# Optimization experiments

Hardware: AMD Instinct MI355X
Metric: run time of the kernel (lower is better)

## Reference

```python
import jax, jax.numpy as jnp
import numpy as np

B, S, D = 8, 2048, 512


def setup_inputs() -> dict:
    key = jax.random.key(0)
    ks = jax.random.split(key, 11)
    scale = 1.0 / np.sqrt(D)
    inp = {"x": jax.random.normal(ks[0], (B, S, D), dtype=jnp.float32)}
    names = ["q", "k", "v", "g", "o"]
    for i, n in enumerate(names):
        inp[f"W{n}"] = jax.random.normal(ks[1 + 2 * i], (D, D), dtype=jnp.float32) * scale
        inp[f"b{n}"] = jax.random.normal(ks[2 + 2 * i], (D,), dtype=jnp.float32) * 0.01
    return inp


def reference(x, Wq, bq, Wk, bk, Wv, bv, Wg, bg, Wo, bo):
    # Projections (torch nn.Linear: x @ W.T + b)
    Q = x @ Wq.T + bq            # (B,S,D)
    K = x @ Wk.T + bk
    V = x @ Wv.T + bv
    gamma = jax.nn.sigmoid(x @ Wg.T + bg)

    # Recurrent linear-attention scan over time.
    # State St: (B,D,D); update: St = gamma_t[:, :, None] * St + k_t ⊗ v_t
    # (decay broadcasts along the key/row dimension, matching
    #  gamma_i.transpose(1,2) * S in the torch code)
    def step(St, qkvg):
        q_t, k_t, v_t, g_t = qkvg           # each (B,D)
        St = g_t[:, :, None] * St + k_t[:, :, None] * v_t[:, None, :]
        out_t = jnp.einsum('bd,bde->be', q_t, St)  # q_i @ S
        return St, out_t

    S0 = jnp.zeros((B, D, D), dtype=x.dtype)
    # time-major inputs for scan: (S,B,D)
    seq = (Q.transpose(1, 0, 2), K.transpose(1, 0, 2),
           V.transpose(1, 0, 2), gamma.transpose(1, 0, 2))
    _, outs = jax.lax.scan(step, S0, seq)   # outs: (S,B,D)
    O = outs.transpose(1, 0, 2)             # (B,S,D)
    return O @ Wo.T + bo
```

## Files before the change

### kernel.cpp

```cpp
#include <hip/hip_runtime.h>
#include <hip/hip_bf16.h>
#include <stdint.h>


#define B_ 8
#define S_ 2048
#define D_ 512
#define M_ (B_ * S_)
#define NSUB 64
#define SUBL 32
#define NSUP 8
#define SUPL 256

typedef __bf16 bf16x8 __attribute__((ext_vector_type(8)));
typedef float f32x4 __attribute__((ext_vector_type(4)));

__device__ __forceinline__ float bflo(uint32_t u){ return __uint_as_float(u<<16); }
__device__ __forceinline__ float bfhi(uint32_t u){ return __uint_as_float(u&0xffff0000u); }
__device__ __forceinline__ uint16_t f2bf(float f){
    uint32_t u = __float_as_uint(f);
    return (uint16_t)((u + 0x7fffu + ((u>>16)&1u)) >> 16);
}
__device__ __forceinline__ uint32_t pack2bf(float a, float b){
    return (uint32_t)f2bf(a) | ((uint32_t)f2bf(b)<<16);
}
__device__ __forceinline__ void gload16(const void* g, void* l){
    __builtin_amdgcn_global_load_lds(
        (const __attribute__((address_space(1))) uint32_t*)g,
        (__attribute__((address_space(3))) uint32_t*)l, 16, 0, 0);
}

__global__ __launch_bounds__(256) void conv_x(const float* __restrict__ in,
                                              uint16_t* __restrict__ out){
    const size_t i = ((size_t)blockIdx.x*256 + threadIdx.x)*8;
    float4 a = *(const float4*)&in[i];
    float4 b = *(const float4*)&in[i+4];
    uint4 o; o.x=pack2bf(a.x,a.y); o.y=pack2bf(a.z,a.w); o.z=pack2bf(b.x,b.y); o.w=pack2bf(b.z,b.w);
    *(uint4*)&out[i] = o;
}
__global__ __launch_bounds__(256) void conv_w(const float* w0, const float* w1, const float* w2,
                                              const float* w3, const float* w4,
                                              uint16_t* __restrict__ out){
    const float* ws[5] = {w0,w1,w2,w3,w4};
    const float* in = ws[blockIdx.y];
    uint16_t* o = out + (size_t)blockIdx.y*D_*D_;
    const size_t i = ((size_t)blockIdx.x*256 + threadIdx.x)*8;
    float4 a = *(const float4*)&in[i];
    float4 b = *(const float4*)&in[i+4];
    uint4 u; u.x=pack2bf(a.x,a.y); u.y=pack2bf(a.z,a.w); u.z=pack2bf(b.x,b.y); u.w=pack2bf(b.z,b.w);
    *(uint4*)&o[i] = u;
}

__global__ __launch_bounds__(256) void proj4(const uint16_t* __restrict__ A,
                                             const uint16_t* __restrict__ Wb,
                                             const float* __restrict__ bq_,
                                             const float* __restrict__ bk_,
                                             const float* __restrict__ bv_,
                                             const float* __restrict__ bg_,
                                             uint16_t* __restrict__ Qb,
                                             uint16_t* __restrict__ Kb,
                                             uint16_t* __restrict__ VT,
                                             float* __restrict__ Gf)
{
    __shared__ __attribute__((aligned(16))) uint16_t SM[17472];
    uint16_t* As = SM;
    uint16_t* Bs = SM + 8192;
    const int tid = threadIdx.x, wave = tid>>6, lane = tid&63;
    const int m0 = blockIdx.x*128, n0 = blockIdx.y*128;
    const int wr = (wave>>1)*64, wc = (wave&1)*64;
    const int fr = lane&15, fq = lane>>4;
    const int sect = blockIdx.y >> 2;
    const int n0c = n0 & 511;
    f32x4 acc[4][4] = {};

    for (int k0 = 0; k0 < D_; k0 += 64) {
        __syncthreads();
#pragma unroll
        for (int i = 0; i < 4; ++i) {
            const int c = i*256 + tid;
            const int row = c>>3, kc = ((c&7) ^ (row&7))*8;
            const int ldsb = (i*256 + wave*64)*8;
            gload16(&A [(size_t)(m0+row)*D_ + k0 + kc], &As[ldsb]);
            gload16(&Wb[(size_t)(n0+row)*D_ + k0 + kc], &Bs[ldsb]);
        }
        __syncthreads();
#pragma unroll
        for (int kk = 0; kk < 64; kk += 32) {
            const int sc = (kk + fq*8) ^ ((fr&7)<<3);
            bf16x8 af[4], bf[4];
#pragma unroll
            for (int m = 0; m < 4; ++m) af[m] = *(const bf16x8*)&As[(wr+m*16+fr)*64 + sc];
#pragma unroll
            for (int n = 0; n < 4; ++n) bf[n] = *(const bf16x8*)&Bs[(wc+n*16+fr)*64 + sc];
            if (sect == 2) {
#pragma unroll
                for (int m = 0; m < 4; ++m)
#pragma unroll
                    for (int n = 0; n < 4; ++n)
                        acc[m][n] = __builtin_amdgcn_mfma_f32_16x16x32_bf16(bf[n], af[m], acc[m][n], 0,0,0);
            } else {
#pragma unroll
                for (int m = 0; m < 4; ++m)
#pragma unroll
                    for (int n = 0; n < 4; ++n)
                        acc[m][n] = __builtin_amdgcn_mfma_f32_16x16x32_bf16(af[m], bf[n], acc[m][n], 0,0,0);
            }
        }
    }
    __syncthreads();

    if (sect == 3) {
        float (*L32)[68] = (float(*)[68])SM;
#pragma unroll
        for (int h = 0; h < 2; ++h) {
            if (wc == h*64) {
#pragma unroll
                for (int n = 0; n < 4; ++n) {
                    const float bvv = bg_[n0c + wc + n*16 + fr];
#pragma unroll
                    for (int m = 0; m < 4; ++m)
#pragma unroll
                        for (int q = 0; q < 4; ++q)
                            L32[wr + m*16 + fq*4 + q][n*16 + fr] =
                                1.f/(1.f + expf(-(acc[m][n][q] + bvv)));
                }
            }
            __syncthreads();
#pragma unroll
            for (int it = 0; it < 8; ++it) {
                const int r = it*16 + (tid>>4), c4 = (tid&15)*4;
                *(uint4*)&Gf[(size_t)(m0+r)*D_ + n0c + h*64 + c4] = *(uint4*)&L32[r][c4];
            }
            __syncthreads();
        }
    } else {
        uint16_t (*L)[136] = (uint16_t(*)[136])SM;
        const float* bias = (sect==0) ? bq_ : (sect==1) ? bk_ : bv_;
        if (sect == 2) {
#pragma unroll
            for (int n = 0; n < 4; ++n)
#pragma unroll
                for (int q = 0; q < 4; ++q) {
                    const int dvl = wc + n*16 + fq*4 + q;
                    const float bvv = bias[n0c + dvl];
#pragma unroll
                    for (int m = 0; m < 4; ++m)
                        L[dvl][wr + m*16 + fr] = f2bf(acc[m][n][q] + bvv);
                }
        } else {
#pragma unroll
            for (int n = 0; n < 4; ++n) {
                const int cl = wc + n*16 + fr;
                const float bvv = bias[n0c + cl];
#pragma unroll
                for (int m = 0; m < 4; ++m)
#pragma unroll
                    for (int q = 0; q < 4; ++q)
                        L[wr + m*16 + fq*4 + q][cl] = f2bf(acc[m][n][q] + bvv);
            }
        }
        __syncthreads();
        const int bb = m0 >> 11, t0 = m0 & 2047;
#pragma unroll
        for (int it = 0; it < 8; ++it) {
            const int r = it*16 + (tid>>4), c8 = (tid&15)*8;
            uint4 v = *(uint4*)&L[r][c8];
            if (sect == 0)      *(uint4*)&Qb[(size_t)(m0+r)*D_ + n0c + c8] = v;
            else if (sect == 1) *(uint4*)&Kb[(size_t)(m0+r)*D_ + n0c + c8] = v;
            else                *(uint4*)&VT[((size_t)bb*D_ + n0c + r)*S_ + t0 + c8] = v;
        }
    }
}

__global__ __launch_bounds__(256) void mfma_gemm(const uint16_t* __restrict__ A,
                                                 const uint16_t* __restrict__ Wt,
                                                 const float* __restrict__ bias,
                                                 float* __restrict__ out)
{
    __shared__ __attribute__((aligned(16))) uint16_t SM[17472];
    uint16_t* As = SM;
    uint16_t* Bs = SM + 8192;
    const int tid = threadIdx.x, wave = tid>>6, lane = tid&63;
    const int m0 = blockIdx.x*128, n0 = blockIdx.y*128;
    const int wr = (wave>>1)*64, wc = (wave&1)*64;
    const int fr = lane&15, fq = lane>>4;
    f32x4 acc[4][4] = {};

    for (int k0 = 0; k0 < D_; k0 += 64) {
        __syncthreads();
#pragma unroll
        for (int i = 0; i < 4; ++i) {
            const int c = i*256 + tid;
            const int row = c>>3, kc = ((c&7) ^ (row&7))*8;
            const int ldsb = (i*256 + wave*64)*8;
            gload16(&A [(size_t)(m0+row)*D_ + k0 + kc], &As[ldsb]);
            gload16(&Wt[(size_t)(n0+row)*D_ + k0 + kc], &Bs[ldsb]);
        }
        __syncthreads();
#pragma unroll
        for (int kk = 0; kk < 64; kk += 32) {
            const int sc = (kk + fq*8) ^ ((fr&7)<<3);
            bf16x8 af[4], bf[4];
#pragma unroll
            for (int m = 0; m < 4; ++m) af[m] = *(const bf16x8*)&As[(wr+m*16+fr)*64 + sc];
#pragma unroll
            for (int n = 0; n < 4; ++n) bf[n] = *(const bf16x8*)&Bs[(wc+n*16+fr)*64 + sc];
#pragma unroll
            for (int m = 0; m < 4; ++m)
#pragma unroll
                for (int n = 0; n < 4; ++n)
                    acc[m][n] = __builtin_amdgcn_mfma_f32_16x16x32_bf16(af[m], bf[n], acc[m][n], 0,0,0);
        }
    }
    __syncthreads();
    float (*L32)[68] = (float(*)[68])SM;
#pragma unroll
    for (int h = 0; h < 2; ++h) {
        if (wc == h*64) {
#pragma unroll
            for (int n = 0; n < 4; ++n) {
                const float bvv = bias[n0 + wc + n*16 + fr];
#pragma unroll
                for (int m = 0; m < 4; ++m)
#pragma unroll
                    for (int q = 0; q < 4; ++q)
                        L32[wr + m*16 + fq*4 + q][n*16 + fr] = acc[m][n][q] + bvv;
            }
        }
        __syncthreads();
#pragma unroll
        for (int it = 0; it < 8; ++it) {
            const int r = it*16 + (tid>>4), c4 = (tid&15)*4;
            *(uint4*)&out[(size_t)(m0+r)*D_ + n0 + h*64 + c4] = *(uint4*)&L32[r][c4];
        }
        __syncthreads();
    }
}

__global__ __launch_bounds__(256) void prep(const float* __restrict__ Gf,
                                            uint16_t* __restrict__ Qb,
                                            uint16_t* __restrict__ Kb,
                                            uint16_t* __restrict__ KT,
                                            float* __restrict__ T)
{
    const int sub = blockIdx.x, b = blockIdx.y;
    const int tid = threadIdx.x;
    const int dk0 = tid*2;
    const size_t rowbase = ((size_t)b*S_ + sub*SUBL)*D_;
    const float*    gp = Gf + rowbase + dk0;
    uint16_t*       qp = Qb + rowbase + dk0;
    uint16_t*       kp = Kb + rowbase + dk0;

    float mu0 = 1.f, mu1 = 1.f;
    uint32_t ksave[SUBL];
#pragma unroll
    for (int t = 0; t < SUBL; ++t) {
        const float2   g  = *(const float2*)(gp + (size_t)t*D_);
        const uint32_t qu = *(const uint32_t*)(qp + (size_t)t*D_);
        const uint32_t ku = *(const uint32_t*)(kp + (size_t)t*D_);
        mu0 = fmaxf(mu0*g.x, 1e-30f);
        mu1 = fmaxf(mu1*g.y, 1e-30f);
        const float r0 = __builtin_amdgcn_rcpf(mu0);
        const float r1 = __builtin_amdgcn_rcpf(mu1);
        *(uint32_t*)(qp + (size_t)t*D_) = pack2bf(bflo(qu)*mu0, bfhi(qu)*mu1);
        const uint32_t kw = pack2bf(bflo(ku)*r0, bfhi(ku)*r1);
        *(uint32_t*)(kp + (size_t)t*D_) = kw;
        ksave[t] = kw;
    }
    T[((size_t)b*NSUB + sub)*D_ + dk0]     = mu0;
    T[((size_t)b*NSUB + sub)*D_ + dk0 + 1] = mu1;

    uint16_t* d0 = &KT[((size_t)b*D_ + dk0)*S_ + sub*SUBL];
    uint16_t* d1 = d0 + S_;
#pragma unroll
    for (int q4 = 0; q4 < 4; ++q4) {
        uint4 lo, hi;
        lo.x = (ksave[q4*8+0]&0xffffu) | (ksave[q4*8+1]<<16);
        lo.y = (ksave[q4*8+2]&0xffffu) | (ksave[q4*8+3]<<16);
        lo.z = (ksave[q4*8+4]&0xffffu) | (ksave[q4*8+5]<<16);
        lo.w = (ksave[q4*8+6]&0xffffu) | (ksave[q4*8+7]<<16);
        hi.x = (ksave[q4*8+0]>>16) | (ksave[q4*8+1]&0xffff0000u);
        hi.y = (ksave[q4*8+2]>>16) | (ksave[q4*8+3]&0xffff0000u);
        hi.z = (ksave[q4*8+4]>>16) | (ksave[q4*8+5]&0xffff0000u);
        hi.w = (ksave[q4*8+6]>>16) | (ksave[q4*8+7]&0xffff0000u);
        *(uint4*)&d0[q4*8] = lo;
        *(uint4*)&d1[q4*8] = hi;
    }
}

__global__ __launch_bounds__(512) void tables(const float* __restrict__ T,
                                              float* __restrict__ Pre,
                                              float* __restrict__ Suf,
                                              float* __restrict__ Lam)
{
    const int b = blockIdx.x, dk = threadIdx.x;
    for (int sp = 0; sp < NSUP; ++sp) {
        float run = 1.f;
#pragma unroll
        for (int m = 0; m < 8; ++m) {
            Pre[((size_t)b*NSUB + sp*8+m)*D_ + dk] = run;
            run *= T[((size_t)b*NSUB + sp*8+m)*D_ + dk];
        }
        Lam[((size_t)b*NSUP + sp)*D_ + dk] = run;
        float rs = 1.f;
#pragma unroll
        for (int m = 7; m >= 0; --m) {
            rs *= T[((size_t)b*NSUB + sp*8+m)*D_ + dk];
            Suf[((size_t)b*NSUB + sp*8+m)*D_ + dk] = rs;
        }
    }
}

__device__ __forceinline__ int swz(int r, int c){ return r*D_ + (c ^ ((r&7)<<3)); }

__global__ __launch_bounds__(256) void pairsA(const uint16_t* __restrict__ Qt,
                                              const uint16_t* __restrict__ Kh,
                                              const float* __restrict__ T,
                                              uint16_t* __restrict__ P)
{
    __shared__ __attribute__((aligned(16))) uint16_t qs[SUBL*D_];
    __shared__ __attribute__((aligned(16))) uint16_t ks[SUBL*D_];
    __shared__ float D_lds[D_];
    const int bx = blockIdx.x, sp = blockIdx.y, b = blockIdx.z;
    const int tid = threadIdx.x, wave = tid>>6, lane = tid&63;
    const int fr = lane&15, fq = lane>>4;
    const int mq = wave>>1, nq = wave&1;
    const int dkA = tid*2, dkB = tid*2+1;

    for (int ii = 0; ii < 2; ++ii) {
        const int i = ii ? 7-bx : bx;
        const size_t qrow = (size_t)b*S_ + sp*SUPL + i*SUBL;
        const size_t prow = ((size_t)(b*NSUP + sp)*SUPL + i*SUBL);

#pragma unroll
        for (int z = 0; z < 8; ++z) {
            int ch = z*256 + tid, r = ch>>6, c = (ch&63)*8;
            *(uint4*)&qs[swz(r,c)] = *(const uint4*)&Qt[(qrow + r)*D_ + c];
            *(uint4*)&ks[swz(r,c)] = *(const uint4*)&Kh[(qrow + r)*D_ + c];
        }
        float d0 = 1.f, d1 = 1.f;

        for (int j = i; j >= 0; --j) {
            if (j < i) {
                d0 *= T[((size_t)b*NSUB + sp*8 + j)*D_ + dkA];
                d1 *= T[((size_t)b*NSUB + sp*8 + j)*D_ + dkB];
                D_lds[dkA] = d0; D_lds[dkB] = d1;
                __syncthreads();
#pragma unroll
                for (int z = 0; z < 8; ++z) {
                    int ch = z*256 + tid, r = ch>>6, c = (ch&63)*8;
                    uint4 u = *(const uint4*)&Kh[((size_t)b*S_ + sp*SUPL + j*SUBL + r)*D_ + c];
                    uint4 o;
                    o.x = pack2bf(bflo(u.x)*D_lds[c+0], bfhi(u.x)*D_lds[c+1]);
                    o.y = pack2bf(bflo(u.y)*D_lds[c+2], bfhi(u.y)*D_lds[c+3]);
                    o.z = pack2bf(bflo(u.z)*D_lds[c+4], bfhi(u.z)*D_lds[c+5]);
                    o.w = pack2bf(bflo(u.w)*D_lds[c+6], bfhi(u.w)*D_lds[c+7]);
                    *(uint4*)&ks[swz(r,c)] = o;
                }
            }
            __syncthreads();
            f32x4 a0 = {}, a1 = {}, a2 = {}, a3 = {};
#pragma unroll
            for (int kk = 0; kk < 512; kk += 128) {
                bf16x8 q0 = *(const bf16x8*)&qs[swz(mq*16+fr, kk      + fq*8)];
                bf16x8 k0 = *(const bf16x8*)&ks[swz(nq*16+fr, kk      + fq*8)];
                bf16x8 q1 = *(const bf16x8*)&qs[swz(mq*16+fr, kk + 32 + fq*8)];
                bf16x8 k1 = *(const bf16x8*)&ks[swz(nq*16+fr, kk + 32 + fq*8)];
                bf16x8 q2 = *(const bf16x8*)&qs[swz(mq*16+fr, kk + 64 + fq*8)];
                bf16x8 k2 = *(const bf16x8*)&ks[swz(nq*16+fr, kk + 64 + fq*8)];
                bf16x8 q3 = *(const bf16x8*)&qs[swz(mq*16+fr, kk + 96 + fq*8)];
                bf16x8 k3 = *(const bf16x8*)&ks[swz(nq*16+fr, kk + 96 + fq*8)];
                a0 = __builtin_amdgcn_mfma_f32_16x16x32_bf16(q0, k0, a0, 0,0,0);
                a1 = __builtin_amdgcn_mfma_f32_16x16x32_bf16(q1, k1, a1, 0,0,0);
                a2 = __builtin_amdgcn_mfma_f32_16x16x32_bf16(q2, k2, a2, 0,0,0);
                a3 = __builtin_amdgcn_mfma_f32_16x16x32_bf16(q3, k3, a3, 0,0,0);
            }
            const int ul = nq*16 + fr;
#pragma unroll
            for (int q_ = 0; q_ < 4; ++q_) {
                const int tl = mq*16 + fq*4 + q_;
                float v = a0[q_] + a1[q_] + a2[q_] + a3[q_];
                if (j == i && ul > tl) v = 0.f;
                P[(prow + tl)*SUPL + j*SUBL + ul] = f2bf(v);
            }
            __syncthreads();
        }
    }
}

__global__ __launch_bounds__(256) void dsgemm(const uint16_t* __restrict__ VT,
                                              const uint16_t* __restrict__ KT,
                                              const float* __restrict__ Suf,
                                              uint16_t* __restrict__ Sst)
{
    __shared__ __attribute__((aligned(16))) uint16_t As[128][40];
    __shared__ __attribute__((aligned(16))) uint16_t Bs[128][40];
    const int tile = blockIdx.x, c = blockIdx.y, b = blockIdx.z;
    const int m0 = (tile&3)*128, n0 = (tile>>2)*128;
    const int tid = threadIdx.x, wave = tid>>6, lane = tid&63;
    const int wr = (wave>>1)*64, wc = (wave&1)*64;
    const int fr = lane&15, fq = lane>>4;
    f32x4 acc[4][4] = {};

    for (int j = 0; j < 8; ++j) {
        const int t0 = c*SUPL + j*SUBL;
        __syncthreads();
#pragma unroll
        for (int ch = tid; ch < 512; ch += 256) {
            int row = ch>>2, tc = (ch&3)*8;
            *(uint4*)&As[row][tc] = *(const uint4*)&VT[((size_t)b*D_ + m0+row)*S_ + t0 + tc];
        }
#pragma unroll
        for (int ch = tid; ch < 512; ch += 256) {
            int row = ch>>2, tc = (ch&3)*8;
            uint4 u = *(const uint4*)&KT[((size_t)b*D_ + n0+row)*S_ + t0 + tc];
            float sf = Suf[((size_t)b*NSUB + c*8 + j)*D_ + n0 + row];
            uint4 o;
            o.x = pack2bf(bflo(u.x)*sf, bfhi(u.x)*sf);
            o.y = pack2bf(bflo(u.y)*sf, bfhi(u.y)*sf);
            o.z = pack2bf(bflo(u.z)*sf, bfhi(u.z)*sf);
            o.w = pack2bf(bflo(u.w)*sf, bfhi(u.w)*sf);
            *(uint4*)&Bs[row][tc] = o;
        }
        __syncthreads();
        bf16x8 af[4], bf[4];
#pragma unroll
        for (int m = 0; m < 4; ++m) af[m] = *(const bf16x8*)&As[wr+m*16+fr][fq*8];
#pragma unroll
        for (int n = 0; n < 4; ++n) bf[n] = *(const bf16x8*)&Bs[wc+n*16+fr][fq*8];
#pragma unroll
        for (int m = 0; m < 4; ++m)
#pragma unroll
            for (int n = 0; n < 4; ++n)
                acc[m][n] = __builtin_amdgcn_mfma_f32_16x16x32_bf16(af[m], bf[n], acc[m][n], 0,0,0);
    }
#pragma unroll
    for (int n = 0; n < 4; ++n) {
        const int dk = n0 + wc + n*16 + fr;
#pragma unroll
        for (int m = 0; m < 4; ++m)
#pragma unroll
            for (int q = 0; q < 4; ++q) {
                const int dv = m0 + wr + m*16 + fq*4 + q;
                Sst[(((size_t)c*B_ + b)*D_ + dv)*D_ + dk] = f2bf(acc[m][n][q]);
            }
    }
}

__global__ __launch_bounds__(256) void scanfix(uint16_t* __restrict__ Sst,
                                               const float* __restrict__ Lam)
{
    const int id = blockIdx.x*256 + threadIdx.x;
    const int g = id & 63, dv = (id>>6) & 511, b = id >> 15;
    const int dk = g*8;
    float s[8];
    {
        uint4 u = *(const uint4*)&Sst[(((size_t)0*B_ + b)*D_ + dv)*D_ + dk];
        s[0]=bflo(u.x); s[1]=bfhi(u.x); s[2]=bflo(u.y); s[3]=bfhi(u.y);
        s[4]=bflo(u.z); s[5]=bfhi(u.z); s[6]=bflo(u.w); s[7]=bfhi(u.w);
    }
    for (int c = 1; c < 7; ++c) {
        const size_t bs = (((size_t)c*B_ + b)*D_ + dv)*D_ + dk;
        uint4 d = *(const uint4*)&Sst[bs];
        float4 l0 = *(const float4*)&Lam[((size_t)b*NSUP + c)*D_ + dk];
        float4 l1 = *(const float4*)&Lam[((size_t)b*NSUP + c)*D_ + dk + 4];
        s[0] = l0.x*s[0] + bflo(d.x); s[1] = l0.y*s[1] + bfhi(d.x);
        s[2] = l0.z*s[2] + bflo(d.y); s[3] = l0.w*s[3] + bfhi(d.y);
        s[4] = l1.x*s[4] + bflo(d.z); s[5] = l1.y*s[5] + bfhi(d.z);
        s[6] = l1.z*s[6] + bflo(d.w); s[7] = l1.w*s[7] + bfhi(d.w);
        uint4 o;
        o.x = pack2bf(s[0],s[1]); o.y = pack2bf(s[2],s[3]);
        o.z = pack2bf(s[4],s[5]); o.w = pack2bf(s[6],s[7]);
        *(uint4*)&Sst[bs] = o;
    }
}

__global__ __launch_bounds__(256) void bigout(const uint16_t* __restrict__ Qt,
                                              const float* __restrict__ Pre,
                                              const uint16_t* __restrict__ Sst,
                                              const uint16_t* __restrict__ Pb,
                                              const uint16_t* __restrict__ VT,
                                              uint16_t* __restrict__ O)
{
    __shared__ __attribute__((aligned(16))) uint16_t SM[17472];
    __shared__ float PreL[4*512];
    uint16_t* As = SM;
    uint16_t* Bs = SM + 8192;
    const int m0 = blockIdx.x*128, n0 = blockIdx.y*128;
    const int b = blockIdx.z>>3, sp = blockIdx.z&7;
    const int tid = threadIdx.x, wave = tid>>6, lane = tid&63;
    const int wr = (wave>>1)*64, wc = (wave&1)*64;
    const int fr = lane&15, fq = lane>>4;
    const int i0 = m0>>5;

#pragma unroll
    for (int z = 0; z < 8; ++z) {
        int idx = z*256 + tid;
        PreL[idx] = Pre[((size_t)b*NSUB + sp*8 + i0 + (idx>>9))*D_ + (idx&511)];
    }
    f32x4 acc[4][4] = {};
    const int kt0 = (sp == 0) ? 8 : 0;
    for (int kt = kt0; kt < 12; ++kt) {
        __syncthreads();
        if (kt < 8) {
            const int k0 = kt*64;
#pragma unroll
            for (int z = 0; z < 4; ++z) {
                int ch = z*256 + tid, r = ch>>3, cc = (ch&7)*8;
                uint4 u = *(const uint4*)&Qt[((size_t)b*S_ + sp*SUPL + m0 + r)*D_ + k0 + cc];
                const float* pr = &PreL[((r>>5)<<9) + k0 + cc];
                uint4 o;
                o.x = pack2bf(bflo(u.x)*pr[0], bfhi(u.x)*pr[1]);
                o.y = pack2bf(bflo(u.y)*pr[2], bfhi(u.y)*pr[3]);
                o.z = pack2bf(bflo(u.z)*pr[4], bfhi(u.z)*pr[5]);
                o.w = pack2bf(bflo(u.w)*pr[6], bfhi(u.w)*pr[7]);
                *(uint4*)&As[r*64 + (cc ^ ((r&7)<<3))] = o;
            }
#pragma unroll
            for (int z = 0; z < 4; ++z) {
                int ch = z*256 + tid, row = ch>>3, kc = ((ch&7) ^ (row&7))*8;
                int ldsb = (z*256 + wave*64)*8;
                gload16(&Sst[(((size_t)(sp-1)*B_ + b)*D_ + n0 + row)*D_ + k0 + kc], &Bs[ldsb]);
            }
        } else {
            const int u0 = (kt-8)*64;
#pragma unroll
            for (int z = 0; z < 4; ++z) {
                int ch = z*256 + tid, row = ch>>3, kc = ((ch&7) ^ (row&7))*8;
                int ldsb = (z*256 + wave*64)*8;
                gload16(&Pb[((size_t)(b*NSUP + sp)*SUPL + m0 + row)*SUPL + u0 + kc], &As[ldsb]);
                gload16(&VT[((size_t)b*D_ + n0 + row)*S_ + sp*SUPL + u0 + kc], &Bs[ldsb]);
            }
        }
        __syncthreads();
#pragma unroll
        for (int kk = 0; kk < 64; kk += 32) {
            const int sc = (kk + fq*8) ^ ((fr&7)<<3);
            bf16x8 af[4], bf[4];
#pragma unroll
            for (int m = 0; m < 4; ++m) af[m] = *(const bf16x8*)&As[(wr+m*16+fr)*64 + sc];
#pragma unroll
            for (int n = 0; n < 4; ++n) bf[n] = *(const bf16x8*)&Bs[(wc+n*16+fr)*64 + sc];
#pragma unroll
            for (int m = 0; m < 4; ++m)
#pragma unroll
                for (int n = 0; n < 4; ++n)
                    acc[m][n] = __builtin_amdgcn_mfma_f32_16x16x32_bf16(af[m], bf[n], acc[m][n], 0,0,0);
        }
    }
    __syncthreads();
    uint16_t (*L)[136] = (uint16_t(*)[136])SM;
#pragma unroll
    for (int n = 0; n < 4; ++n) {
        const int cl = wc + n*16 + fr;
#pragma unroll
        for (int m = 0; m < 4; ++m)
#pragma unroll
            for (int q = 0; q < 4; ++q)
                L[wr + m*16 + fq*4 + q][cl] = f2bf(acc[m][n][q]);
    }
    __syncthreads();
#pragma unroll
    for (int it = 0; it < 8; ++it) {
        const int r = it*16 + (tid>>4), c8 = (tid&15)*8;
        *(uint4*)&O[((size_t)b*S_ + sp*SUPL + m0 + r)*D_ + n0 + c8] = *(uint4*)&L[r][c8];
    }
}

extern "C" void kernel_launch(void* const* d_in, const int* in_sizes, int n_in,
                              void* d_out, int out_size, void* d_ws, size_t ws_size,
                              hipStream_t stream)
{
    (void)in_sizes; (void)n_in; (void)out_size; (void)ws_size;
    const float* x  = (const float*)d_in[0];
    const float* Wq = (const float*)d_in[1];  const float* bq = (const float*)d_in[2];
    const float* Wk = (const float*)d_in[3];  const float* bk = (const float*)d_in[4];
    const float* Wv = (const float*)d_in[5];  const float* bv = (const float*)d_in[6];
    const float* Wg = (const float*)d_in[7];  const float* bg = (const float*)d_in[8];
    const float* Wo = (const float*)d_in[9];  const float* bo = (const float*)d_in[10];

    char* w = (char*)d_ws;
    const size_t MD2 = (size_t)M_*D_*2;
    uint16_t* Wb = (uint16_t*)w;                       w += 5*(size_t)D_*D_*2;
    uint16_t* xb = (uint16_t*)w;                       w += MD2;
    uint16_t* Qb = (uint16_t*)w;                       w += MD2;
    uint16_t* Kb = (uint16_t*)w;                       w += MD2;
    uint16_t* KT = (uint16_t*)w;                       w += MD2;
    uint16_t* VT = (uint16_t*)w;                       w += MD2;
    float*    Gf = (float*)w;                          w += (size_t)M_*D_*4;
    uint16_t* Sst = (uint16_t*)w;                      w += (size_t)7*B_*D_*D_*2;
    uint16_t* Pb  = (uint16_t*)w;                      w += (size_t)B_*NSUP*SUPL*SUPL*2;
    float*    T   = (float*)w;                         w += (size_t)B_*NSUB*D_*4;
    float*    Pre = (float*)w;                         w += (size_t)B_*NSUB*D_*4;
    float*    Suf = (float*)w;                         w += (size_t)B_*NSUB*D_*4;
    float*    Lam = (float*)w;                         w += (size_t)B_*NSUP*D_*4;

    hipMemsetAsync(Pb, 0, (size_t)B_*NSUP*SUPL*SUPL*2, stream);

    conv_x<<<dim3(M_*D_/2048), 256, 0, stream>>>(x, xb);
    conv_w<<<dim3(D_*D_/2048, 5), 256, 0, stream>>>(Wq, Wk, Wv, Wg, Wo, Wb);

    proj4<<<dim3(M_/128, 16), 256, 0, stream>>>(xb, Wb, bq, bk, bv, bg, Qb, Kb, VT, Gf);

    prep<<<dim3(NSUB, B_), 256, 0, stream>>>(Gf, Qb, Kb, KT, T);
    tables<<<dim3(B_), 512, 0, stream>>>(T, Pre, Suf, Lam);

    pairsA<<<dim3(4, NSUP, B_), 256, 0, stream>>>(Qb, Kb, T, Pb);
    dsgemm<<<dim3(16, 7, B_), 256, 0, stream>>>(VT, KT, Suf, Sst);
    scanfix<<<dim3(1024), 256, 0, stream>>>(Sst, Lam);

    bigout<<<dim3(2, 4, B_*NSUP), 256, 0, stream>>>(Qb, Pre, Sst, Pb, VT, xb);

    mfma_gemm<<<dim3(M_/128, D_/128), 256, 0, stream>>>(xb, Wb + 4*(size_t)D_*D_, bo, (float*)d_out);
}
```

Baseline: 218.1 us.

## Double-buffer GEMM LDS stages, store gamma as bf16, parallelize pairsA and tables

Adds double-buffered LDS staging with prefetch of the next k-tile to the proj4, output GEMM, dsgemm and bigout kernels, which removes one barrier per iteration and overlaps loads with MFMA. The gate activations are now written as bf16 instead of fp32, halving that traffic, and prep reads them as bf16. pairsA launches one block per (i,j) sub-block pair instead of looping serially, and tables runs one block per superchunk instead of per batch. The Pb memset is dropped; bigout instead zeroes the upper-triangle A fragments itself. In exchange the gate loses precision, and the decay products feeding the scan are computed from rounded values.

```diff
diff --git a/kernel.cpp b/kernel.cpp
--- a/kernel.cpp
+++ b/kernel.cpp
@@ -60,11 +60,9 @@
                                              uint16_t* __restrict__ Qb,
                                              uint16_t* __restrict__ Kb,
                                              uint16_t* __restrict__ VT,
-                                             float* __restrict__ Gf)
-{
-    __shared__ __attribute__((aligned(16))) uint16_t SM[17472];
-    uint16_t* As = SM;
-    uint16_t* Bs = SM + 8192;
+                                             uint16_t* __restrict__ Gb)
+{
+    __shared__ __attribute__((aligned(16))) uint16_t SM[2][16384];
     const int tid = threadIdx.x, wave = tid>>6, lane = tid&63;
     const int m0 = blockIdx.x*128, n0 = blockIdx.y*128;
     const int wr = (wave>>1)*64, wc = (wave&1)*64;
@@ -73,102 +71,90 @@
     const int n0c = n0 & 511;
     f32x4 acc[4][4] = {};
 
-    for (int k0 = 0; k0 < D_; k0 += 64) {
-        __syncthreads();
+    auto STAGE = [&](int kt, int p){
+        const int k0 = kt*64;
 #pragma unroll
         for (int i = 0; i < 4; ++i) {
             const int c = i*256 + tid;
             const int row = c>>3, kc = ((c&7) ^ (row&7))*8;
             const int ldsb = (i*256 + wave*64)*8;
-            gload16(&A [(size_t)(m0+row)*D_ + k0 + kc], &As[ldsb]);
-            gload16(&Wb[(size_t)(n0+row)*D_ + k0 + kc], &Bs[ldsb]);
-        }
-        __syncthreads();
+            gload16(&A [(size_t)(m0+row)*D_ + k0 + kc], &SM[p][ldsb]);
+            gload16(&Wb[(size_t)(n0+row)*D_ + k0 + kc], &SM[p][8192+ldsb]);
+        }
+    };
+    auto COMP = [&](int p){
 #pragma unroll
         for (int kk = 0; kk < 64; kk += 32) {
             const int sc = (kk + fq*8) ^ ((fr&7)<<3);
-            bf16x8 af[4], bf[4];
-#pragma unroll
-            for (int m = 0; m < 4; ++m) af[m] = *(const bf16x8*)&As[(wr+m*16+fr)*64 + sc];
-#pragma unroll
-            for (int n = 0; n < 4; ++n) bf[n] = *(const bf16x8*)&Bs[(wc+n*16+fr)*64 + sc];
+            bf16x8 af[4], bfv[4];
+#pragma unroll
+            for (int m = 0; m < 4; ++m) af[m]  = *(const bf16x8*)&SM[p][(wr+m*16+fr)*64 + sc];
+#pragma unroll
+            for (int n = 0; n < 4; ++n) bfv[n] = *(const bf16x8*)&SM[p][8192+(wc+n*16+fr)*64 + sc];
             if (sect == 2) {
 #pragma unroll
                 for (int m = 0; m < 4; ++m)
 #pragma unroll
                     for (int n = 0; n < 4; ++n)
-                        acc[m][n] = __builtin_amdgcn_mfma_f32_16x16x32_bf16(bf[n], af[m], acc[m][n], 0,0,0);
+                        acc[m][n] = __builtin_amdgcn_mfma_f32_16x16x32_bf16(bfv[n], af[m], acc[m][n], 0,0,0);
             } else {
 #pragma unroll
                 for (int m = 0; m < 4; ++m)
 #pragma unroll
                     for (int n = 0; n < 4; ++n)
-                        acc[m][n] = __builtin_amdgcn_mfma_f32_16x16x32_bf16(af[m], bf[n], acc[m][n], 0,0,0);
+                        acc[m][n] = __builtin_amdgcn_mfma_f32_16x16x32_bf16(af[m], bfv[n], acc[m][n], 0,0,0);
             }
         }
-    }
-    __syncthreads();
-
-    if (sect == 3) {
-        float (*L32)[68] = (float(*)[68])SM;
-#pragma unroll
-        for (int h = 0; h < 2; ++h) {
-            if (wc == h*64) {
-#pragma unroll
-                for (int n = 0; n < 4; ++n) {
-                    const float bvv = bg_[n0c + wc + n*16 + fr];
-#pragma unroll
-                    for (int m = 0; m < 4; ++m)
-#pragma unroll
-                        for (int q = 0; q < 4; ++q)
-                            L32[wr + m*16 + fq*4 + q][n*16 + fr] =
-                                1.f/(1.f + expf(-(acc[m][n][q] + bvv)));
+    };
+
+    STAGE(0, 0);
+    __syncthreads();
+    int p = 0;
+    for (int kt = 0; kt < 8; ++kt) {
+        if (kt < 7) STAGE(kt+1, p^1);
+        COMP(p);
+        __syncthreads();
+        p ^= 1;
+    }
+
+    uint16_t (*L)[136] = (uint16_t(*)[136])&SM[0][0];
+    const float* bias = (sect==0) ? bq_ : (sect==1) ? bk_ : (sect==2) ? bv_ : bg_;
+    if (sect == 2) {
+#pragma unroll
+        for (int n = 0; n < 4; ++n)
+#pragma unroll
+            for (int q = 0; q < 4; ++q) {
+                const int dvl = wc + n*16 + fq*4 + q;
+                const float bvv = bias[n0c + dvl];
+#pragma unroll
+                for (int m = 0; m < 4; ++m)
+                    L[dvl][wr + m*16 + fr] = f2bf(acc[m][n][q] + bvv);
+            }
+    } else {
+#pragma unroll
+        for (int n = 0; n < 4; ++n) {
+            const int cl = wc + n*16 + fr;
+            const float bvv = bias[n0c + cl];
+#pragma unroll
+            for (int m = 0; m < 4; ++m)
+#pragma unroll
+                for (int q = 0; q < 4; ++q) {
+                    float c = acc[m][n][q] + bvv;
+                    if (sect == 3) c = 1.f/(1.f + expf(-c));
+                    L[wr + m*16 + fq*4 + q][cl] = f2bf(c);
                 }
-            }
-            __syncthreads();
-#pragma unroll
-            for (int it = 0; it < 8; ++it) {
-                const int r = it*16 + (tid>>4), c4 = (tid&15)*4;
-                *(uint4*)&Gf[(size_t)(m0+r)*D_ + n0c + h*64 + c4] = *(uint4*)&L32[r][c4];
-            }
-            __syncthreads();
-        }
-    } else {
-        uint16_t (*L)[136] = (uint16_t(*)[136])SM;
-        const float* bias = (sect==0) ? bq_ : (sect==1) ? bk_ : bv_;
-        if (sect == 2) {
-#pragma unroll
-            for (int n = 0; n < 4; ++n)
-#pragma unroll
-                for (int q = 0; q < 4; ++q) {
-                    const int dvl = wc + n*16 + fq*4 + q;
-                    const float bvv = bias[n0c + dvl];
-#pragma unroll
-                    for (int m = 0; m < 4; ++m)
-                        L[dvl][wr + m*16 + fr] = f2bf(acc[m][n][q] + bvv);
-                }
-        } else {
-#pragma unroll
-            for (int n = 0; n < 4; ++n) {
-                const int cl = wc + n*16 + fr;
-                const float bvv = bias[n0c + cl];
-#pragma unroll
-                for (int m = 0; m < 4; ++m)
-#pragma unroll
-                    for (int q = 0; q < 4; ++q)
-                        L[wr + m*16 + fq*4 + q][cl] = f2bf(acc[m][n][q] + bvv);
-            }
-        }
-        __syncthreads();
-        const int bb = m0 >> 11, t0 = m0 & 2047;
-#pragma unroll
-        for (int it = 0; it < 8; ++it) {
-            const int r = it*16 + (tid>>4), c8 = (tid&15)*8;
-            uint4 v = *(uint4*)&L[r][c8];
-            if (sect == 0)      *(uint4*)&Qb[(size_t)(m0+r)*D_ + n0c + c8] = v;
-            else if (sect == 1) *(uint4*)&Kb[(size_t)(m0+r)*D_ + n0c + c8] = v;
-            else                *(uint4*)&VT[((size_t)bb*D_ + n0c + r)*S_ + t0 + c8] = v;
-        }
+        }
+    }
+    __syncthreads();
+    const int bb = m0 >> 11, t0 = m0 & 2047;
+#pragma unroll
+    for (int it = 0; it < 8; ++it) {
+        const int r = it*16 + (tid>>4), c8 = (tid&15)*8;
+        uint4 v = *(uint4*)&L[r][c8];
+        if (sect == 0)      *(uint4*)&Qb[(size_t)(m0+r)*D_ + n0c + c8] = v;
+        else if (sect == 1) *(uint4*)&Kb[(size_t)(m0+r)*D_ + n0c + c8] = v;
+        else if (sect == 3) *(uint4*)&Gb[(size_t)(m0+r)*D_ + n0c + c8] = v;
+        else                *(uint4*)&VT[((size_t)bb*D_ + n0c + r)*S_ + t0 + c8] = v;
     }
 }
 
@@ -177,43 +163,52 @@
                                                  const float* __restrict__ bias,
                                                  float* __restrict__ out)
 {
-    __shared__ __attribute__((aligned(16))) uint16_t SM[17472];
-    uint16_t* As = SM;
-    uint16_t* Bs = SM + 8192;
+    __shared__ __attribute__((aligned(16))) uint16_t SM[2][16384];
     const int tid = threadIdx.x, wave = tid>>6, lane = tid&63;
     const int m0 = blockIdx.x*128, n0 = blockIdx.y*128;
     const int wr = (wave>>1)*64, wc = (wave&1)*64;
     const int fr = lane&15, fq = lane>>4;
     f32x4 acc[4][4] = {};
 
-    for (int k0 = 0; k0 < D_; k0 += 64) {
-        __syncthreads();
+    auto STAGE = [&](int kt, int p){
+        const int k0 = kt*64;
 #pragma unroll
         for (int i = 0; i < 4; ++i) {
             const int c = i*256 + tid;
             const int row = c>>3, kc = ((c&7) ^ (row&7))*8;
             const int ldsb = (i*256 + wave*64)*8;
-            gload16(&A [(size_t)(m0+row)*D_ + k0 + kc], &As[ldsb]);
-            gload16(&Wt[(size_t)(n0+row)*D_ + k0 + kc], &Bs[ldsb]);
-        }
-        __syncthreads();
+            gload16(&A [(size_t)(m0+row)*D_ + k0 + kc], &SM[p][ldsb]);
+            gload16(&Wt[(size_t)(n0+row)*D_ + k0 + kc], &SM[p][8192+ldsb]);
+        }
+    };
+    auto COMP = [&](int p){
 #pragma unroll
         for (int kk = 0; kk < 64; kk += 32) {
             const int sc = (kk + fq*8) ^ ((fr&7)<<3);
-            bf16x8 af[4], bf[4];
-#pragma unroll
-            for (int m = 0; m < 4; ++m) af[m] = *(const bf16x8*)&As[(wr+m*16+fr)*64 + sc];
-#pragma unroll
-            for (int n = 0; n < 4; ++n) bf[n] = *(const bf16x8*)&Bs[(wc+n*16+fr)*64 + sc];
+            bf16x8 af[4], bfv[4];
+#pragma unroll
+            for (int m = 0; m < 4; ++m) af[m]  = *(const bf16x8*)&SM[p][(wr+m*16+fr)*64 + sc];
+#pragma unroll
+            for (int n = 0; n < 4; ++n) bfv[n] = *(const bf16x8*)&SM[p][8192+(wc+n*16+fr)*64 + sc];
 #pragma unroll
             for (int m = 0; m < 4; ++m)
 #pragma unroll
                 for (int n = 0; n < 4; ++n)
-                    acc[m][n] = __builtin_amdgcn_mfma_f32_16x16x32_bf16(af[m], bf[n], acc[m][n], 0,0,0);
-        }
-    }
-    __syncthreads();
-    float (*L32)[68] = (float(*)[68])SM;
+                    acc[m][n] = __builtin_amdgcn_mfma_f32_16x16x32_bf16(af[m], bfv[n], acc[m][n], 0,0,0);
+        }
+    };
+
+    STAGE(0, 0);
+    __syncthreads();
+    int p = 0;
+    for (int kt = 0; kt < 8; ++kt) {
+        if (kt < 7) STAGE(kt+1, p^1);
+        COMP(p);
+        __syncthreads();
+        p ^= 1;
+    }
+
+    float (*L32)[68] = (float(*)[68])&SM[0][0];
 #pragma unroll
     for (int h = 0; h < 2; ++h) {
         if (wc == h*64) {
@@ -237,7 +232,7 @@
     }
 }
 
-__global__ __launch_bounds__(256) void prep(const float* __restrict__ Gf,
+__global__ __launch_bounds__(256) void prep(const uint16_t* __restrict__ Gb,
                                             uint16_t* __restrict__ Qb,
                                             uint16_t* __restrict__ Kb,
                                             uint16_t* __restrict__ KT,
@@ -247,7 +242,7 @@
     const int tid = threadIdx.x;
     const int dk0 = tid*2;
     const size_t rowbase = ((size_t)b*S_ + sub*SUBL)*D_;
-    const float*    gp = Gf + rowbase + dk0;
+    const uint16_t* gp = Gb + rowbase + dk0;
     uint16_t*       qp = Qb + rowbase + dk0;
     uint16_t*       kp = Kb + rowbase + dk0;
 
@@ -255,11 +250,11 @@
     uint32_t ksave[SUBL];
 #pragma unroll
     for (int t = 0; t < SUBL; ++t) {
-        const float2   g  = *(const float2*)(gp + (size_t)t*D_);
+        const uint32_t g2 = *(const uint32_t*)(gp + (size_t)t*D_);
         const uint32_t qu = *(const uint32_t*)(qp + (size_t)t*D_);
         const uint32_t ku = *(const uint32_t*)(kp + (size_t)t*D_);
-        mu0 = fmaxf(mu0*g.x, 1e-30f);
-        mu1 = fmaxf(mu1*g.y, 1e-30f);
+        mu0 = fmaxf(mu0*bflo(g2), 1e-30f);
+        mu1 = fmaxf(mu1*bfhi(g2), 1e-30f);
         const float r0 = __builtin_amdgcn_rcpf(mu0);
         const float r1 = __builtin_amdgcn_rcpf(mu1);
         *(uint32_t*)(qp + (size_t)t*D_) = pack2bf(bflo(qu)*mu0, bfhi(qu)*mu1);
@@ -293,21 +288,19 @@
                                               float* __restrict__ Suf,
                                               float* __restrict__ Lam)
 {
-    const int b = blockIdx.x, dk = threadIdx.x;
-    for (int sp = 0; sp < NSUP; ++sp) {
-        float run = 1.f;
-#pragma unroll
-        for (int m = 0; m < 8; ++m) {
-            Pre[((size_t)b*NSUB + sp*8+m)*D_ + dk] = run;
-            run *= T[((size_t)b*NSUB + sp*8+m)*D_ + dk];
-        }
-        Lam[((size_t)b*NSUP + sp)*D_ + dk] = run;
-        float rs = 1.f;
-#pragma unroll
-        for (int m = 7; m >= 0; --m) {
-            rs *= T[((size_t)b*NSUB + sp*8+m)*D_ + dk];
-            Suf[((size_t)b*NSUB + sp*8+m)*D_ + dk] = rs;
-        }
+    const int sp = blockIdx.x, b = blockIdx.y, dk = threadIdx.x;
+    float run = 1.f;
+#pragma unroll
+    for (int m = 0; m < 8; ++m) {
+        Pre[((size_t)b*NSUB + sp*8+m)*D_ + dk] = run;
+        run *= T[((size_t)b*NSUB + sp*8+m)*D_ + dk];
+    }
+    Lam[((size_t)b*NSUP + sp)*D_ + dk] = run;
+    float rs = 1.f;
+#pragma unroll
+    for (int m = 7; m >= 0; --m) {
+        rs *= T[((size_t)b*NSUB + sp*8+m)*D_ + dk];
+        Suf[((size_t)b*NSUB + sp*8+m)*D_ + dk] = rs;
     }
 }
 
@@ -321,70 +314,68 @@
     __shared__ __attribute__((aligned(16))) uint16_t qs[SUBL*D_];
     __shared__ __attribute__((aligned(16))) uint16_t ks[SUBL*D_];
     __shared__ float D_lds[D_];
-    const int bx = blockIdx.x, sp = blockIdx.y, b = blockIdx.z;
+    const int idx = blockIdx.x, sp = blockIdx.y, b = blockIdx.z;
+    int i = 0;
+    while (((i+1)*(i+2))/2 <= idx) ++i;
+    const int j = idx - (i*(i+1))/2;
+
     const int tid = threadIdx.x, wave = tid>>6, lane = tid&63;
     const int fr = lane&15, fq = lane>>4;
     const int mq = wave>>1, nq = wave&1;
+    const size_t qrow = (size_t)b*S_ + sp*SUPL + i*SUBL;
+    const size_t krow = (size_t)b*S_ + sp*SUPL + j*SUBL;
+    const size_t prow = ((size_t)(b*NSUP + sp)*SUPL + i*SUBL);
+
+#pragma unroll
+    for (int z = 0; z < 8; ++z) {
+        int ch = z*256 + tid, r = ch>>6, c = (ch&63)*8;
+        *(uint4*)&qs[swz(r,c)] = *(const uint4*)&Qt[(qrow + r)*D_ + c];
+    }
     const int dkA = tid*2, dkB = tid*2+1;
-
-    for (int ii = 0; ii < 2; ++ii) {
-        const int i = ii ? 7-bx : bx;
-        const size_t qrow = (size_t)b*S_ + sp*SUPL + i*SUBL;
-        const size_t prow = ((size_t)(b*NSUP + sp)*SUPL + i*SUBL);
-
-#pragma unroll
-        for (int z = 0; z < 8; ++z) {
-            int ch = z*256 + tid, r = ch>>6, c = (ch&63)*8;
-            *(uint4*)&qs[swz(r,c)] = *(const uint4*)&Qt[(qrow + r)*D_ + c];
-            *(uint4*)&ks[swz(r,c)] = *(const uint4*)&Kh[(qrow + r)*D_ + c];
-        }
-        float d0 = 1.f, d1 = 1.f;
-
-        for (int j = i; j >= 0; --j) {
-            if (j < i) {
-                d0 *= T[((size_t)b*NSUB + sp*8 + j)*D_ + dkA];
-                d1 *= T[((size_t)b*NSUB + sp*8 + j)*D_ + dkB];
-                D_lds[dkA] = d0; D_lds[dkB] = d1;
-                __syncthreads();
-#pragma unroll
-                for (int z = 0; z < 8; ++z) {
-                    int ch = z*256 + tid, r = ch>>6, c = (ch&63)*8;
-                    uint4 u = *(const uint4*)&Kh[((size_t)b*S_ + sp*SUPL + j*SUBL + r)*D_ + c];
-                    uint4 o;
-                    o.x = pack2bf(bflo(u.x)*D_lds[c+0], bfhi(u.x)*D_lds[c+1]);
-                    o.y = pack2bf(bflo(u.y)*D_lds[c+2], bfhi(u.y)*D_lds[c+3]);
-                    o.z = pack2bf(bflo(u.z)*D_lds[c+4], bfhi(u.z)*D_lds[c+5]);
-                    o.w = pack2bf(bflo(u.w)*D_lds[c+6], bfhi(u.w)*D_lds[c+7]);
-                    *(uint4*)&ks[swz(r,c)] = o;
-                }
-            }
-            __syncthreads();
-            f32x4 a0 = {}, a1 = {}, a2 = {}, a3 = {};
-#pragma unroll
-            for (int kk = 0; kk < 512; kk += 128) {
-                bf16x8 q0 = *(const bf16x8*)&qs[swz(mq*16+fr, kk      + fq*8)];
-                bf16x8 k0 = *(const bf16x8*)&ks[swz(nq*16+fr, kk      + fq*8)];
-                bf16x8 q1 = *(const bf16x8*)&qs[swz(mq*16+fr, kk + 32 + fq*8)];
-                bf16x8 k1 = *(const bf16x8*)&ks[swz(nq*16+fr, kk + 32 + fq*8)];
-                bf16x8 q2 = *(const bf16x8*)&qs[swz(mq*16+fr, kk + 64 + fq*8)];
-                bf16x8 k2 = *(const bf16x8*)&ks[swz(nq*16+fr, kk + 64 + fq*8)];
-                bf16x8 q3 = *(const bf16x8*)&qs[swz(mq*16+fr, kk + 96 + fq*8)];
-                bf16x8 k3 = *(const bf16x8*)&ks[swz(nq*16+fr, kk + 96 + fq*8)];
-                a0 = __builtin_amdgcn_mfma_f32_16x16x32_bf16(q0, k0, a0, 0,0,0);
-                a1 = __builtin_amdgcn_mfma_f32_16x16x32_bf16(q1, k1, a1, 0,0,0);
-                a2 = __builtin_amdgcn_mfma_f32_16x16x32_bf16(q2, k2, a2, 0,0,0);
-                a3 = __builtin_amdgcn_mfma_f32_16x16x32_bf16(q3, k3, a3, 0,0,0);
-            }
-            const int ul = nq*16 + fr;
-#pragma unroll
-            for (int q_ = 0; q_ < 4; ++q_) {
-                const int tl = mq*16 + fq*4 + q_;
-                float v = a0[q_] + a1[q_] + a2[q_] + a3[q_];
-                if (j == i && ul > tl) v = 0.f;
-                P[(prow + tl)*SUPL + j*SUBL + ul] = f2bf(v);
-            }
-            __syncthreads();
-        }
+    float d0 = 1.f, d1 = 1.f;
+    for (int m = j; m < i; ++m) {
+        d0 *= T[((size_t)b*NSUB + sp*8 + m)*D_ + dkA];
+        d1 *= T[((size_t)b*NSUB + sp*8 + m)*D_ + dkB];
+    }
+    D_lds[dkA] = d0; D_lds[dkB] = d1;
+    __syncthreads();
+
+#pragma unroll
+    for (int z = 0; z < 8; ++z) {
+        int ch = z*256 + tid, r = ch>>6, c = (ch&63)*8;
+        uint4 u = *(const uint4*)&Kh[(krow + r)*D_ + c];
+        uint4 o;
+        o.x = pack2bf(bflo(u.x)*D_lds[c+0], bfhi(u.x)*D_lds[c+1]);
+        o.y = pack2bf(bflo(u.y)*D_lds[c+2], bfhi(u.y)*D_lds[c+3]);
+        o.z = pack2bf(bflo(u.z)*D_lds[c+4], bfhi(u.z)*D_lds[c+5]);
+        o.w = pack2bf(bflo(u.w)*D_lds[c+6], bfhi(u.w)*D_lds[c+7]);
+        *(uint4*)&ks[swz(r,c)] = o;
+    }
+    __syncthreads();
+
+    f32x4 a0 = {}, a1 = {}, a2 = {}, a3 = {};
+#pragma unroll
+    for (int kk = 0; kk < 512; kk += 128) {
+        bf16x8 q0 = *(const bf16x8*)&qs[swz(mq*16+fr, kk      + fq*8)];
+        bf16x8 k0 = *(const bf16x8*)&ks[swz(nq*16+fr, kk      + fq*8)];
+        bf16x8 q1 = *(const bf16x8*)&qs[swz(mq*16+fr, kk + 32 + fq*8)];
+        bf16x8 k1 = *(const bf16x8*)&ks[swz(nq*16+fr, kk + 32 + fq*8)];
+        bf16x8 q2 = *(const bf16x8*)&qs[swz(mq*16+fr, kk + 64 + fq*8)];
+        bf16x8 k2 = *(const bf16x8*)&ks[swz(nq*16+fr, kk + 64 + fq*8)];
+        bf16x8 q3 = *(const bf16x8*)&qs[swz(mq*16+fr, kk + 96 + fq*8)];
+        bf16x8 k3 = *(const bf16x8*)&ks[swz(nq*16+fr, kk + 96 + fq*8)];
+        a0 = __builtin_amdgcn_mfma_f32_16x16x32_bf16(q0, k0, a0, 0,0,0);
+        a1 = __builtin_amdgcn_mfma_f32_16x16x32_bf16(q1, k1, a1, 0,0,0);
+        a2 = __builtin_amdgcn_mfma_f32_16x16x32_bf16(q2, k2, a2, 0,0,0);
+        a3 = __builtin_amdgcn_mfma_f32_16x16x32_bf16(q3, k3, a3, 0,0,0);
+    }
+    const int ul = nq*16 + fr;
+#pragma unroll
+    for (int q_ = 0; q_ < 4; ++q_) {
+        const int tl = mq*16 + fq*4 + q_;
+        float v = a0[q_] + a1[q_] + a2[q_] + a3[q_];
+        if (i == j && ul > tl) v = 0.f;
+        P[(prow + tl)*SUPL + j*SUBL + ul] = f2bf(v);
     }
 }
 
@@ -393,8 +384,8 @@
                                               const float* __restrict__ Suf,
                                               uint16_t* __restrict__ Sst)
 {
-    __shared__ __attribute__((aligned(16))) uint16_t As[128][40];
-    __shared__ __attribute__((aligned(16))) uint16_t Bs[128][40];
+    __shared__ __attribute__((aligned(16))) uint16_t As[2][128][40];
+    __shared__ __attribute__((aligned(16))) uint16_t Bs[2][128][40];
     const int tile = blockIdx.x, c = blockIdx.y, b = blockIdx.z;
     const int m0 = (tile&3)*128, n0 = (tile>>2)*128;
     const int tid = threadIdx.x, wave = tid>>6, lane = tid&63;
@@ -402,13 +393,12 @@
     const int fr = lane&15, fq = lane>>4;
     f32x4 acc[4][4] = {};
 
-    for (int j = 0; j < 8; ++j) {
+    auto STAGE = [&](int j, int p){
         const int t0 = c*SUPL + j*SUBL;
-        __syncthreads();
 #pragma unroll
         for (int ch = tid; ch < 512; ch += 256) {
             int row = ch>>2, tc = (ch&3)*8;
-            *(uint4*)&As[row][tc] = *(const uint4*)&VT[((size_t)b*D_ + m0+row)*S_ + t0 + tc];
+            *(uint4*)&As[p][row][tc] = *(const uint4*)&VT[((size_t)b*D_ + m0+row)*S_ + t0 + tc];
         }
 #pragma unroll
         for (int ch = tid; ch < 512; ch += 256) {
@@ -420,19 +410,27 @@
             o.y = pack2bf(bflo(u.y)*sf, bfhi(u.y)*sf);
             o.z = pack2bf(bflo(u.z)*sf, bfhi(u.z)*sf);
             o.w = pack2bf(bflo(u.w)*sf, bfhi(u.w)*sf);
-            *(uint4*)&Bs[row][tc] = o;
-        }
-        __syncthreads();
+            *(uint4*)&Bs[p][row][tc] = o;
+        }
+    };
+
+    STAGE(0, 0);
+    __syncthreads();
+    int p = 0;
+    for (int j = 0; j < 8; ++j) {
+        if (j < 7) STAGE(j+1, p^1);
         bf16x8 af[4], bf[4];
 #pragma unroll
-        for (int m = 0; m < 4; ++m) af[m] = *(const bf16x8*)&As[wr+m*16+fr][fq*8];
-#pragma unroll
-        for (int n = 0; n < 4; ++n) bf[n] = *(const bf16x8*)&Bs[wc+n*16+fr][fq*8];
+        for (int m = 0; m < 4; ++m) af[m] = *(const bf16x8*)&As[p][wr+m*16+fr][fq*8];
+#pragma unroll
+        for (int n = 0; n < 4; ++n) bf[n] = *(const bf16x8*)&Bs[p][wc+n*16+fr][fq*8];
 #pragma unroll
         for (int m = 0; m < 4; ++m)
 #pragma unroll
             for (int n = 0; n < 4; ++n)
                 acc[m][n] = __builtin_amdgcn_mfma_f32_16x16x32_bf16(af[m], bf[n], acc[m][n], 0,0,0);
+        __syncthreads();
+        p ^= 1;
     }
 #pragma unroll
     for (int n = 0; n < 4; ++n) {
@@ -482,10 +480,8 @@
                                               const uint16_t* __restrict__ VT,
                                               uint16_t* __restrict__ O)
 {
-    __shared__ __attribute__((aligned(16))) uint16_t SM[17472];
+    __shared__ __attribute__((aligned(16))) uint16_t SM[2][16384];
     __shared__ float PreL[4*512];
-    uint16_t* As = SM;
-    uint16_t* Bs = SM + 8192;
     const int m0 = blockIdx.x*128, n0 = blockIdx.y*128;
     const int b = blockIdx.z>>3, sp = blockIdx.z&7;
     const int tid = threadIdx.x, wave = tid>>6, lane = tid&63;
@@ -499,28 +495,48 @@
         PreL[idx] = Pre[((size_t)b*NSUB + sp*8 + i0 + (idx>>9))*D_ + (idx&511)];
     }
     f32x4 acc[4][4] = {};
-    const int kt0 = (sp == 0) ? 8 : 0;
-    for (int kt = kt0; kt < 12; ++kt) {
-        __syncthreads();
+    uint4 areg[4];
+
+    auto ISSUE_A = [&](int kt){
+        const int k0 = kt*64;
+#pragma unroll
+        for (int z = 0; z < 4; ++z) {
+            int ch = z*256 + tid, r = ch>>3, cc = (ch&7)*8;
+            areg[z] = *(const uint4*)&Qt[((size_t)b*S_ + sp*SUPL + m0 + r)*D_ + k0 + cc];
+        }
+    };
+    auto WRITE_A = [&](int kt, int p){
+        const int k0 = kt*64;
+#pragma unroll
+        for (int z = 0; z < 4; ++z) {
+            int ch = z*256 + tid, r = ch>>3, cc = (ch&7)*8;
+            const float* pr = &PreL[((r>>5)<<9) + k0 + cc];
+            uint4 u = areg[z];
+            uint4 o;
+            o.x = pack2bf(bflo(u.x)*pr[0], bfhi(u.x)*pr[1]);
+            o.y = pack2bf(bflo(u.y)*pr[2], bfhi(u.y)*pr[3]);
+            o.z = pack2bf(bflo(u.z)*pr[4], bfhi(u.z)*pr[5]);
+            o.w = pack2bf(bflo(u.w)*pr[6], bfhi(u.w)*pr[7]);
+            *(uint4*)&SM[p][r*64 + (cc ^ ((r&7)<<3))] = o;
+        }
+    };
+    auto STAGE_A_GL = [&](int kt, int p){
+        const int u0 = (kt-8)*64;
+#pragma unroll
+        for (int z = 0; z < 4; ++z) {
+            int ch = z*256 + tid, row = ch>>3, kc = ((ch&7) ^ (row&7))*8;
+            int ldsb = (z*256 + wave*64)*8;
+            gload16(&Pb[((size_t)(b*NSUP + sp)*SUPL + m0 + row)*SUPL + u0 + kc], &SM[p][ldsb]);
+        }
+    };
+    auto STAGE_B = [&](int kt, int p){
         if (kt < 8) {
             const int k0 = kt*64;
-#pragma unroll
-            for (int z = 0; z < 4; ++z) {
-                int ch = z*256 + tid, r = ch>>3, cc = (ch&7)*8;
-                uint4 u = *(const uint4*)&Qt[((size_t)b*S_ + sp*SUPL + m0 + r)*D_ + k0 + cc];
-                const float* pr = &PreL[((r>>5)<<9) + k0 + cc];
-                uint4 o;
-                o.x = pack2bf(bflo(u.x)*pr[0], bfhi(u.x)*pr[1]);
-                o.y = pack2bf(bflo(u.y)*pr[2], bfhi(u.y)*pr[3]);
-                o.z = pack2bf(bflo(u.z)*pr[4], bfhi(u.z)*pr[5]);
-                o.w = pack2bf(bflo(u.w)*pr[6], bfhi(u.w)*pr[7]);
-                *(uint4*)&As[r*64 + (cc ^ ((r&7)<<3))] = o;
-            }
 #pragma unroll
             for (int z = 0; z < 4; ++z) {
                 int ch = z*256 + tid, row = ch>>3, kc = ((ch&7) ^ (row&7))*8;
                 int ldsb = (z*256 + wave*64)*8;
-                gload16(&Sst[(((size_t)(sp-1)*B_ + b)*D_ + n0 + row)*D_ + k0 + kc], &Bs[ldsb]);
+                gload16(&Sst[(((size_t)(sp-1)*B_ + b)*D_ + n0 + row)*D_ + k0 + kc], &SM[p][8192+ldsb]);
             }
         } else {
             const int u0 = (kt-8)*64;
@@ -528,28 +544,62 @@
             for (int z = 0; z < 4; ++z) {
                 int ch = z*256 + tid, row = ch>>3, kc = ((ch&7) ^ (row&7))*8;
                 int ldsb = (z*256 + wave*64)*8;
-                gload16(&Pb[((size_t)(b*NSUP + sp)*SUPL + m0 + row)*SUPL + u0 + kc], &As[ldsb]);
-                gload16(&VT[((size_t)b*D_ + n0 + row)*S_ + sp*SUPL + u0 + kc], &Bs[ldsb]);
+                gload16(&VT[((size_t)b*D_ + n0 + row)*S_ + sp*SUPL + u0 + kc], &SM[p][8192+ldsb]);
             }
         }
-        __syncthreads();
+    };
+    auto COMP = [&](int p, int kt){
+        const bf16x8 zz = {};
 #pragma unroll
         for (int kk = 0; kk < 64; kk += 32) {
             const int sc = (kk + fq*8) ^ ((fr&7)<<3);
-            bf16x8 af[4], bf[4];
-#pragma unroll
-            for (int m = 0; m < 4; ++m) af[m] = *(const bf16x8*)&As[(wr+m*16+fr)*64 + sc];
-#pragma unroll
-            for (int n = 0; n < 4; ++n) bf[n] = *(const bf16x8*)&Bs[(wc+n*16+fr)*64 + sc];
+            bf16x8 af[4], bfv[4];
+#pragma unroll
+            for (int m = 0; m < 4; ++m) af[m] = *(const bf16x8*)&SM[p][(wr+m*16+fr)*64 + sc];
+            if (kt >= 8) {
+                const int jb = ((kt-8)*64 + kk) >> 5;
+#pragma unroll
+                for (int m = 0; m < 4; ++m) {
+                    const int ib = (m0 + wr + m*16) >> 5;
+                    if (jb > ib) af[m] = zz;
+                }
+            }
+#pragma unroll
+            for (int n = 0; n < 4; ++n) bfv[n] = *(const bf16x8*)&SM[p][8192+(wc+n*16+fr)*64 + sc];
 #pragma unroll
             for (int m = 0; m < 4; ++m)
 #pragma unroll
                 for (int n = 0; n < 4; ++n)
-                    acc[m][n] = __builtin_amdgcn_mfma_f32_16x16x32_bf16(af[m], bf[n], acc[m][n], 0,0,0);
-        }
-    }
-    __syncthreads();
-    uint16_t (*L)[136] = (uint16_t(*)[136])SM;
+                    acc[m][n] = __builtin_amdgcn_mfma_f32_16x16x32_bf16(af[m], bfv[n], acc[m][n], 0,0,0);
+        }
+    };
+
+    const int kt0 = (sp == 0) ? 8 : 0;
+    if (kt0 < 8) {
+        ISSUE_A(kt0);
+        STAGE_B(kt0, 0);
+        __syncthreads();
+        WRITE_A(kt0, 0);
+    } else {
+        STAGE_A_GL(kt0, 0);
+        STAGE_B(kt0, 0);
+    }
+    __syncthreads();
+
+    int p = 0;
+    for (int kt = kt0; kt < 12; ++kt) {
+        const int nxt = kt + 1;
+        if (nxt < 12) {
+            if (nxt < 8) ISSUE_A(nxt); else STAGE_A_GL(nxt, p^1);
+            STAGE_B(nxt, p^1);
+        }
+        COMP(p, kt);
+        if (nxt < 12 && nxt < 8) WRITE_A(nxt, p^1);
+        __syncthreads();
+        p ^= 1;
+    }
+
+    uint16_t (*L)[136] = (uint16_t(*)[136])&SM[0][0];
 #pragma unroll
     for (int n = 0; n < 4; ++n) {
         const int cl = wc + n*16 + fr;
@@ -587,7 +637,7 @@
     uint16_t* Kb = (uint16_t*)w;                       w += MD2;
     uint16_t* KT = (uint16_t*)w;                       w += MD2;
     uint16_t* VT = (uint16_t*)w;                       w += MD2;
-    float*    Gf = (float*)w;                          w += (size_t)M_*D_*4;
+    uint16_t* Gb = (uint16_t*)w;                       w += MD2;
     uint16_t* Sst = (uint16_t*)w;                      w += (size_t)7*B_*D_*D_*2;
     uint16_t* Pb  = (uint16_t*)w;                      w += (size_t)B_*NSUP*SUPL*SUPL*2;
     float*    T   = (float*)w;                         w += (size_t)B_*NSUB*D_*4;
@@ -595,17 +645,15 @@
     float*    Suf = (float*)w;                         w += (size_t)B_*NSUB*D_*4;
     float*    Lam = (float*)w;                         w += (size_t)B_*NSUP*D_*4;
 
-    hipMemsetAsync(Pb, 0, (size_t)B_*NSUP*SUPL*SUPL*2, stream);
-
     conv_x<<<dim3(M_*D_/2048), 256, 0, stream>>>(x, xb);
     conv_w<<<dim3(D_*D_/2048, 5), 256, 0, stream>>>(Wq, Wk, Wv, Wg, Wo, Wb);
 
-    proj4<<<dim3(M_/128, 16), 256, 0, stream>>>(xb, Wb, bq, bk, bv, bg, Qb, Kb, VT, Gf);
-
-    prep<<<dim3(NSUB, B_), 256, 0, stream>>>(Gf, Qb, Kb, KT, T);
-    tables<<<dim3(B_), 512, 0, stream>>>(T, Pre, Suf, Lam);
-
-    pairsA<<<dim3(4, NSUP, B_), 256, 0, stream>>>(Qb, Kb, T, Pb);
+    proj4<<<dim3(M_/128, 16), 256, 0, stream>>>(xb, Wb, bq, bk, bv, bg, Qb, Kb, VT, Gb);
+
+    prep<<<dim3(NSUB, B_), 256, 0, stream>>>(Gb, Qb, Kb, KT, T);
+    tables<<<dim3(NSUP, B_), 512, 0, stream>>>(T, Pre, Suf, Lam);
+
+    pairsA<<<dim3(36, NSUP, B_), 256, 0, stream>>>(Qb, Kb, T, Pb);
     dsgemm<<<dim3(16, 7, B_), 256, 0, stream>>>(VT, KT, Suf, Sst);
     scanfix<<<dim3(1024), 256, 0, stream>>>(Sst, Lam);
 
```

Result: faster. 201.9 us (-7.4%).
